# Kernel optimization log

Hardware: AMD Instinct MI355X
Metric: run time of the kernel (lower is better)

## Reference

```python
import jax, jax.numpy as jnp
import numpy as np
from jax import lax

B, CIN, COUT, N, H, W = 8, 64, 64, 9, 128, 128
KS, PAD = 3, 1
EPS = 1e-5
DN = ('NCHW', 'OIHW', 'NCHW')

def _conv(x, w, b, pad):
    y = lax.conv_general_dilated(x, w, (1, 1), [(pad, pad), (pad, pad)], dimension_numbers=DN)
    return y + b[None, :, None, None]

def setup_inputs() -> dict:
    key = jax.random.key(0)
    ks = jax.random.split(key, 8)
    fan = CIN * KS * KS
    s = 1.0 / np.sqrt(fan)
    return {
        'x': jax.random.normal(ks[0], (B, CIN, H, W), dtype=jnp.float32),
        'kernels_w': jax.random.uniform(ks[1], (N, COUT, CIN, KS, KS), minval=-s, maxval=s, dtype=jnp.float32),
        'kernels_b': jax.random.uniform(ks[2], (N, COUT), minval=-s, maxval=s, dtype=jnp.float32),
        'obs1_w': jax.random.uniform(ks[3], (COUT // 2, CIN, 1, 1), minval=-1/np.sqrt(CIN), maxval=1/np.sqrt(CIN), dtype=jnp.float32),
        'obs1_b': jax.random.uniform(ks[4], (COUT // 2,), minval=-1/np.sqrt(CIN), maxval=1/np.sqrt(CIN), dtype=jnp.float32),
        'obs2_w': jax.random.uniform(ks[5], (N, COUT // 2, 1, 1), minval=-1/np.sqrt(COUT // 2), maxval=1/np.sqrt(COUT // 2), dtype=jnp.float32),
        'obs2_b': jax.random.uniform(ks[6], (N,), minval=-1/np.sqrt(COUT // 2), maxval=1/np.sqrt(COUT // 2), dtype=jnp.float32),
        'gamma': jnp.ones((COUT,), dtype=jnp.float32),
        'beta': jnp.zeros((COUT,), dtype=jnp.float32),
    }

def reference(x, kernels_w, kernels_b, obs1_w, obs1_b, obs2_w, obs2_b, gamma, beta):
    b, _, h, w = x.shape
    # all N path convs as one grouped-output conv: (B, N*COUT, H, W)
    paths = _conv(x, kernels_w.reshape(N * COUT, CIN, KS, KS), kernels_b.reshape(-1), PAD)
    paths = paths.reshape(b, N, COUT, h, w)
    # observer: 1x1 conv -> tanh -> 1x1 conv, scores (B, N, H, W)
    scores = _conv(jnp.tanh(_conv(x, obs1_w, obs1_b, 0)), obs2_w, obs2_b, 0)
    # eval-mode collapse: per-pixel argmax over paths, one-hot weighted sum == gather
    idx = jnp.argmax(scores, axis=1)  # (B, H, W)
    sel = jnp.take_along_axis(paths, idx[:, None, None, :, :], axis=1)[:, 0]  # (B, COUT, H, W)
    out = jax.nn.relu(sel)
    # ModularPhaseNorm2d (assumed instance-norm-style per-channel spatial norm with affine)
    mu = jnp.mean(out, axis=(2, 3), keepdims=True)
    var = jnp.var(out, axis=(2, 3), keepdims=True)
    y = (out - mu) * lax.rsqrt(var + EPS)
    return y * gamma[None, :, None, None] + beta[None, :, None, None]
```

## Files before the change

### kernel.cpp

```cpp
#include <hip/hip_runtime.h>
#include <hip/hip_bf16.h>
#include <stdint.h>

#define B_    8
#define CIN   64
#define COUT  64
#define NPATH 9
#define H_    128
#define W_    128
#define HW    16384
#define PTOT  131072
#define NBIN  72
#define CHUNK 64
#define NBLK  256

typedef float  f32x4  __attribute__((ext_vector_type(4)));
typedef __bf16 bf16x8 __attribute__((ext_vector_type(8)));
typedef short  short8 __attribute__((ext_vector_type(8)));
typedef unsigned short ushort4v __attribute__((ext_vector_type(4)));

__device__ __forceinline__ short f2bf(float f) {
    __bf16 b = (__bf16)f;
    return __builtin_bit_cast(short, b);
}
__device__ __forceinline__ float bf2f(unsigned short u) {
    unsigned v = ((unsigned)u) << 16;
    return __builtin_bit_cast(float, v);
}

__global__ void k_pre(const float* __restrict__ x,
                      const float* __restrict__ w1, const float* __restrict__ b1,
                      const float* __restrict__ w2, const float* __restrict__ b2,
                      const float* __restrict__ kw,
                      unsigned* __restrict__ gcnt, unsigned* __restrict__ lists,
                      unsigned short* __restrict__ Xb,
                      unsigned short* __restrict__ WbF) {
    int t = threadIdx.x;
    if (blockIdx.x >= 512) {
        int ob = ((int)blockIdx.x - 512) * 4096 + t * 16;
        #pragma unroll
        for (int j = 0; j < 16; ++j) {
            int o = ob + j;
            int jj   = o & 7;
            int lane = (o >> 3) & 63;
            int f    = (o >> 9) & 3;
            int rest = o >> 11;
            int s    = rest % 18;
            int n    = rest / 18;
            int c    = f * 16 + (lane & 15);
            int kg   = lane >> 4;
            int ci   = ((s & 1) << 5) + (kg << 3) + jj;
            int tap  = s >> 1;
            WbF[o] = (unsigned short)f2bf(kw[((n * 64 + c) * 64 + ci) * 9 + tap]);
        }
        return;
    }
    __shared__ float sw1[2048];
    __shared__ float sw2[288];
    __shared__ float sb1[32];
    __shared__ float sb2[9];
    __shared__ unsigned scnt[NBIN];
    __shared__ unsigned sbase[NBIN];
    #pragma unroll
    for (int i = 0; i < 8; ++i) sw1[t + i * 256] = w1[t + i * 256];
    for (int i = t; i < 288; i += 256) sw2[i] = w2[i];
    if (t < 32) sb1[t] = b1[t];
    if (t < 9)  sb2[t] = b2[t];
    if (t < NBIN) scnt[t] = 0u;
    __syncthreads();

    int p  = blockIdx.x * 256 + t;
    int b  = p >> 14;
    const float* xp = x + (size_t)b * 64 * HW + (p & 16383);
    float xv[64];
    #pragma unroll
    for (int ci = 0; ci < 64; ++ci) xv[ci] = xp[ci * HW];

    #pragma unroll
    for (int j = 0; j < 8; ++j) {
        short8 v;
        #pragma unroll
        for (int q = 0; q < 8; ++q) v[q] = f2bf(xv[j * 8 + q]);
        *(short8*)(Xb + (((size_t)p) << 6) + j * 8) = v;
    }

    float s[9];
    #pragma unroll
    for (int nn = 0; nn < 9; ++nn) s[nn] = sb2[nn];

    for (int j = 0; j < 32; ++j) {
        float a = sb1[j];
        const float4* wv = (const float4*)&sw1[j * 64];
        #pragma unroll
        for (int q = 0; q < 16; ++q) {
            float4 v = wv[q];
            a += xv[q*4+0]*v.x + xv[q*4+1]*v.y + xv[q*4+2]*v.z + xv[q*4+3]*v.w;
        }
        float hsig = tanhf(a);
        #pragma unroll
        for (int nn = 0; nn < 9; ++nn) s[nn] += hsig * sw2[nn * 32 + j];
    }
    float best = s[0]; int bi = 0;
    #pragma unroll
    for (int nn = 1; nn < 9; ++nn) if (s[nn] > best) { best = s[nn]; bi = nn; }

    int bin = bi * 8 + b;
    unsigned rank = atomicAdd(&scnt[bin], 1u);
    __syncthreads();
    if (t < NBIN && scnt[t]) sbase[t] = atomicAdd(&gcnt[t], scnt[t]);
    __syncthreads();
    lists[bin * 16384 + sbase[bin] + rank] = (unsigned)p;
}

__global__ void k_prefix(const unsigned* __restrict__ gcnt,
                         unsigned long long* __restrict__ chunkinfo,
                         unsigned* __restrict__ ctot) {
    __shared__ unsigned st[NBIN + 1];
    int t = threadIdx.x;
    if (t == 0) {
        unsigned acc = 0;
        for (int bin = 0; bin < NBIN; ++bin) {
            st[bin] = acc;
            acc += (gcnt[bin] + (CHUNK - 1u)) / CHUNK;
        }
        st[NBIN] = acc;
        *ctot = acc;
    }
    __syncthreads();
    if (t < NBIN) {
        unsigned c0 = st[t], cnt = gcnt[t];
        unsigned nch = (cnt + (CHUNK - 1u)) / CHUNK;
        for (unsigned k = 0; k < nch; ++k)
            chunkinfo[c0 + k] = ((unsigned long long)t << 32)
                              | ((unsigned long long)cnt << 16)
                              | (unsigned long long)(k * CHUNK);
    }
}

__global__ __launch_bounds__(512, 2) void k_conv(
        const unsigned short* __restrict__ Xb, const unsigned short* __restrict__ WbF,
        const float* __restrict__ kb, const unsigned* __restrict__ lists,
        const unsigned long long* __restrict__ chunkinfo, const unsigned* __restrict__ ctot,
        unsigned short* __restrict__ Yc, float* __restrict__ sums) {
    __shared__ char blds[2][73728];
    int t = threadIdx.x;
    int wid = t >> 6, lane = t & 63, kg = lane >> 4, l15 = lane & 15;
    int f = wid & 3, gh = wid >> 2;
    int spx = t >> 3;
    int sq8 = ((t & 7) ^ (spx & 7)) * 8;

    unsigned C = *ctot;
    unsigned bid = (blockIdx.x & 7) * 32 + (blockIdx.x >> 3);
    unsigned c0 = (bid * C) / NBLK, c1 = ((bid + 1) * C) / NBLK;
    if (c0 >= c1) return;

    #define STAGE9(P, BUF) do {                                                   \
        unsigned p_ = (P);                                                        \
        int h_ = (int)((p_ >> 7) & 127u), w_ = (int)(p_ & 127u);                  \
        unsigned pb_ = p_ & ~16383u;                                              \
        _Pragma("unroll")                                                         \
        for (int k_ = 0; k_ < 9; ++k_) {                                          \
            int dh_ = k_ / 3 - 1, dw_ = k_ % 3 - 1;                               \
            int h2_ = min(max(h_ + dh_, 0), 127);                                 \
            int w2_ = min(max(w_ + dw_, 0), 127);                                 \
            const unsigned short* src_ =                                          \
                Xb + ((size_t)(pb_ | (unsigned)((h2_ << 7) + w2_)) << 6) + sq8;   \
            __builtin_amdgcn_global_load_lds(                                     \
                (const __attribute__((address_space(1))) unsigned int*)src_,      \
                (__attribute__((address_space(3))) unsigned int*)((BUF) + k_ * 8192 + t * 16), \
                16, 0, 0);                                                        \
        }                                                                         \
    } while (0)

    unsigned long long info = chunkinfo[c0];
    int bin  = (int)(info >> 32);
    int cnt  = (int)((info >> 16) & 0xFFFFu);
    int base = (int)(info & 0xFFFFu);
    int n = bin >> 3, b = bin & 7;

    short8 wv[18];
    #pragma unroll
    for (int s = 0; s < 18; ++s)
        wv[s] = *(const short8*)(WbF + n * 36864 + ((s * 4 + f) * 64 + lane) * 8);
    f32x4 bias = *(const f32x4*)(kb + n * 64 + f * 16 + kg * 4);

    unsigned pc0 = lists[bin * 16384 + min(base + gh * 32 + l15,      cnt - 1)];
    unsigned pc1 = lists[bin * 16384 + min(base + gh * 32 + 16 + l15, cnt - 1)];
    { unsigned ps = lists[bin * 16384 + min(base + spx, cnt - 1)];
      STAGE9(ps, blds[0]); }

    int cur = 0;
    float s1[4] = {0.f,0.f,0.f,0.f}, s2[4] = {0.f,0.f,0.f,0.f};

    for (unsigned c = c0; c < c1; ++c) {
        bool last = (c + 1 >= c1);
        int bin_n = bin, cnt_n = cnt, base_n = base;
        unsigned pn0 = 0, pn1 = 0;
        if (!last) {
            unsigned long long in2 = chunkinfo[c + 1];
            bin_n  = (int)(in2 >> 32);
            cnt_n  = (int)((in2 >> 16) & 0xFFFFu);
            base_n = (int)(in2 & 0xFFFFu);
            pn0 = lists[bin_n * 16384 + min(base_n + gh * 32 + l15,      cnt_n - 1)];
            pn1 = lists[bin_n * 16384 + min(base_n + gh * 32 + 16 + l15, cnt_n - 1)];
            { unsigned ps = lists[bin_n * 16384 + min(base_n + spx, cnt_n - 1)];
              STAGE9(ps, blds[cur ^ 1]); }
            asm volatile("s_waitcnt vmcnt(11)" ::: "memory");
        } else {
            asm volatile("s_waitcnt vmcnt(0)" ::: "memory");
        }
        __builtin_amdgcn_sched_barrier(0);
        __builtin_amdgcn_s_barrier();

        int v0 = (base + gh * 32 + l15)      < cnt ? 1 : 0;
        int v1 = (base + gh * 32 + 16 + l15) < cnt ? 1 : 0;
        int inb0 = 0, inb1 = 0;
        {
            int h0 = (int)((pc0 >> 7) & 127u), w0 = (int)(pc0 & 127u);
            int h1 = (int)((pc1 >> 7) & 127u), w1 = (int)(pc1 & 127u);
            #pragma unroll
            for (int tap = 0; tap < 9; ++tap) {
                int dh = tap / 3 - 1, dw = tap % 3 - 1;
                if ((unsigned)(h0 + dh) < 128u && (unsigned)(w0 + dw) < 128u) inb0 |= (1 << tap);
                if ((unsigned)(h1 + dh) < 128u && (unsigned)(w1 + dw) < 128u) inb1 |= (1 << tap);
            }
            inb0 = v0 ? inb0 : 0;
            inb1 = v1 ? inb1 : 0;
        }

        f32x4 acc0 = (f32x4)0.0f, acc1 = (f32x4)0.0f;
        const short8 zero8 = (short8)0;
        const char* bufc = blds[cur];
        #pragma unroll
        for (int s = 0; s < 18; ++s) {
            const int tap = s >> 1, half = s & 1;
            bf16x8 af = __builtin_bit_cast(bf16x8, wv[s]);
            const int q = (((half << 2) + kg) ^ (l15 & 7)) * 16;
            {
                int px = gh * 32 + l15;
                short8 braw = *(const short8*)(bufc + tap * 8192 + px * 128 + q);
                short8 sel = ((inb0 >> tap) & 1) ? braw : zero8;
                acc0 = __builtin_amdgcn_mfma_f32_16x16x32_bf16(
                           af, __builtin_bit_cast(bf16x8, sel), acc0, 0, 0, 0);
            }
            {
                int px = gh * 32 + 16 + l15;
                short8 braw = *(const short8*)(bufc + tap * 8192 + px * 128 + q);
                short8 sel = ((inb1 >> tap) & 1) ? braw : zero8;
                acc1 = __builtin_amdgcn_mfma_f32_16x16x32_bf16(
                           af, __builtin_bit_cast(bf16x8, sel), acc1, 0, 0, 0);
            }
        }

        {
            f32x4 o0, o1;
            #pragma unroll
            for (int r = 0; r < 4; ++r) {
                o0[r] = fmaxf(acc0[r] + bias[r], 0.0f);
                o1[r] = fmaxf(acc1[r] + bias[r], 0.0f);
            }
            if (v0) {
                ushort4v u;
                #pragma unroll
                for (int r = 0; r < 4; ++r) u[r] = (unsigned short)f2bf(o0[r]);
                *(ushort4v*)(Yc + (((size_t)pc0) << 6) + f * 16 + kg * 4) = u;
            }
            if (v1) {
                ushort4v u;
                #pragma unroll
                for (int r = 0; r < 4; ++r) u[r] = (unsigned short)f2bf(o1[r]);
                *(ushort4v*)(Yc + (((size_t)pc1) << 6) + f * 16 + kg * 4) = u;
            }
            #pragma unroll
            for (int r = 0; r < 4; ++r) {
                float a = v0 ? o0[r] : 0.0f, bb = v1 ? o1[r] : 0.0f;
                s1[r] += a + bb;
                s2[r] += a * a + bb * bb;
            }
        }

        if (!last && bin_n != bin) {
            float f1[4], f2[4];
            #pragma unroll
            for (int r = 0; r < 4; ++r) { f1[r] = s1[r]; f2[r] = s2[r]; s1[r] = 0.f; s2[r] = 0.f; }
            #pragma unroll
            for (int m = 1; m < 16; m <<= 1) {
                #pragma unroll
                for (int r = 0; r < 4; ++r) {
                    f1[r] += __shfl_xor(f1[r], m, 64);
                    f2[r] += __shfl_xor(f2[r], m, 64);
                }
            }
            if (l15 == 0) {
                #pragma unroll
                for (int r = 0; r < 4; ++r) {
                    int ch = f * 16 + kg * 4 + r;
                    atomicAdd(&sums[b * 64 + ch],       f1[r]);
                    atomicAdd(&sums[512 + b * 64 + ch], f2[r]);
                }
            }
            n = bin_n >> 3; b = bin_n & 7;
            #pragma unroll
            for (int s = 0; s < 18; ++s)
                wv[s] = *(const short8*)(WbF + n * 36864 + ((s * 4 + f) * 64 + lane) * 8);
            bias = *(const f32x4*)(kb + n * 64 + f * 16 + kg * 4);
        }
        bin = bin_n; cnt = cnt_n; base = base_n; pc0 = pn0; pc1 = pn1;
        cur ^= 1;
        __builtin_amdgcn_s_barrier();
    }

    #pragma unroll
    for (int m = 1; m < 16; m <<= 1) {
        #pragma unroll
        for (int r = 0; r < 4; ++r) {
            s1[r] += __shfl_xor(s1[r], m, 64);
            s2[r] += __shfl_xor(s2[r], m, 64);
        }
    }
    if (l15 == 0) {
        #pragma unroll
        for (int r = 0; r < 4; ++r) {
            int ch = f * 16 + kg * 4 + r;
            atomicAdd(&sums[b * 64 + ch],       s1[r]);
            atomicAdd(&sums[512 + b * 64 + ch], s2[r]);
        }
    }
    #undef STAGE9
}

__global__ void k_final(const unsigned short* __restrict__ Yc, const float* __restrict__ sums,
                        const float* __restrict__ gamma, const float* __restrict__ beta,
                        float* __restrict__ out) {
    __shared__ float ld[128][66];
    __shared__ float smu[64], srs[64], sg[64], sb[64];
    int t = threadIdx.x;
    int b = blockIdx.y, hw0 = blockIdx.x * 128;
    if (t < 64) {
        float mu = sums[b * 64 + t] * (1.0f / HW);
        float vr = sums[512 + b * 64 + t] * (1.0f / HW) - mu * mu;
        smu[t] = mu;
        srs[t] = rsqrtf(fmaxf(vr, 0.0f) + 1e-5f);
        sg[t] = gamma[t]; sb[t] = beta[t];
    }
    int i = t >> 1, half = t & 1;
    const short8* row = (const short8*)(Yc + (((size_t)(b * HW + hw0 + i)) << 6) + half * 32);
    #pragma unroll
    for (int q = 0; q < 4; ++q) {
        short8 v = row[q];
        #pragma unroll
        for (int j = 0; j < 8; ++j)
            ld[i][half * 32 + q * 8 + j] = bf2f((unsigned short)v[j]);
    }
    __syncthreads();
    #pragma unroll
    for (int rep = 0; rep < 32; ++rep) {
        int idx = rep * 256 + t;
        int c = idx >> 7, j = idx & 127;
        float v = (ld[j][c] - smu[c]) * srs[c] * sg[c] + sb[c];
        out[(((size_t)b * 64 + c) << 14) + hw0 + j] = v;
    }
}

extern "C" void kernel_launch(void* const* d_in, const int* in_sizes, int n_in,
                              void* d_out, int out_size, void* d_ws, size_t ws_size,
                              hipStream_t stream) {
    const float* x    = (const float*)d_in[0];
    const float* kw   = (const float*)d_in[1];
    const float* kb   = (const float*)d_in[2];
    const float* w1   = (const float*)d_in[3];
    const float* b1   = (const float*)d_in[4];
    const float* w2   = (const float*)d_in[5];
    const float* b2   = (const float*)d_in[6];
    const float* gam  = (const float*)d_in[7];
    const float* bet  = (const float*)d_in[8];
    float* out = (float*)d_out;

    char* ws = (char*)d_ws;
    unsigned* gcnt      = (unsigned*)(ws + 0);
    unsigned* ctot      = (unsigned*)(ws + 512);
    float*    sums      = (float*)   (ws + 4096);
    unsigned long long* chunkinfo = (unsigned long long*)(ws + 16384);
    unsigned* lists     = (unsigned*)(ws + 65536);
    unsigned short* Yc  = (unsigned short*)(ws + 5308416);
    unsigned short* Xb  = (unsigned short*)(ws + 22085632);
    unsigned short* WbF = (unsigned short*)(ws + 38862848);

    hipMemsetAsync(ws, 0, 8192, stream);
    k_pre<<<593, 256, 0, stream>>>(x, w1, b1, w2, b2, kw, gcnt, lists, Xb, WbF);
    k_prefix<<<1, 256, 0, stream>>>(gcnt, chunkinfo, ctot);
    k_conv<<<NBLK, 512, 0, stream>>>(Xb, WbF, kb, lists, chunkinfo, ctot, Yc, sums);
    k_final<<<dim3(128, 8), 256, 0, stream>>>(Yc, sums, gam, bet, out);
}
```

Baseline: 98.10 us.

## Stage x through LDS in pre-pass, halve conv chunk size and deepen prefetch

The pre-pass now loads a 512-pixel tile of x into LDS with async global-to-LDS copies and has each thread process two pixels. It also swaps tanhf for an exp2-based approximation. The conv kernel halves the chunk size to 32 pixels and doubles the block count to 512. It halves the LDS buffers to allow four blocks per CU, splits the 9-tap staging across two thread halves, and prefetches chunk metadata two chunks ahead. The intent is better occupancy, more load balance across bins and more latency hiding, at the cost of more weight reloads on bin changes and a fast tanh that could flip argmax ties.

Result: slower. 108.6 us (+10.7%).

```diff
diff --git a/kernel.cpp b/kernel.cpp
--- a/kernel.cpp
+++ b/kernel.cpp
@@ -11,8 +11,9 @@
 #define HW    16384
 #define PTOT  131072
 #define NBIN  72
-#define CHUNK 64
-#define NBLK  256
+#define CHUNK 32
+#define NBLK  512
+#define MAXCHUNK 8192
 
 typedef float  f32x4  __attribute__((ext_vector_type(4)));
 typedef __bf16 bf16x8 __attribute__((ext_vector_type(8)));
@@ -27,8 +28,13 @@
     unsigned v = ((unsigned)u) << 16;
     return __builtin_bit_cast(float, v);
 }
-
-__global__ void k_pre(const float* __restrict__ x,
+__device__ __forceinline__ float fast_tanh(float a) {
+    float e = __builtin_amdgcn_exp2f(a * 2.885390081777927f);
+    return 1.0f - 2.0f / (e + 1.0f);
+}
+
+__global__ __launch_bounds__(256) void k_pre(
+                      const float* __restrict__ x,
                       const float* __restrict__ w1, const float* __restrict__ b1,
                       const float* __restrict__ w2, const float* __restrict__ b2,
                       const float* __restrict__ kw,
@@ -36,8 +42,8 @@
                       unsigned short* __restrict__ Xb,
                       unsigned short* __restrict__ WbF) {
     int t = threadIdx.x;
-    if (blockIdx.x >= 512) {
-        int ob = ((int)blockIdx.x - 512) * 4096 + t * 16;
+    if (blockIdx.x >= 256) {
+        int ob = ((int)blockIdx.x - 256) * 4096 + t * 16;
         #pragma unroll
         for (int j = 0; j < 16; ++j) {
             int o = ob + j;
@@ -55,12 +61,29 @@
         }
         return;
     }
+    __shared__ float tile[64 * 512];
     __shared__ float sw1[2048];
     __shared__ float sw2[288];
     __shared__ float sb1[32];
     __shared__ float sb2[9];
     __shared__ unsigned scnt[NBIN];
     __shared__ unsigned sbase[NBIN];
+    int wid = t >> 6, lane = t & 63;
+    int px0 = blockIdx.x * 512;
+    int hwb = px0 & 16383;
+    int b = blockIdx.x >> 5;
+
+    #pragma unroll
+    for (int k = 0; k < 16; ++k) {
+        int ch = wid * 16 + k;
+        const float* src = x + (((size_t)(b * 64 + ch)) << 14) + hwb;
+        #pragma unroll
+        for (int hf = 0; hf < 2; ++hf)
+            __builtin_amdgcn_global_load_lds(
+                (const __attribute__((address_space(1))) unsigned int*)(src + hf * 256 + lane * 4),
+                (__attribute__((address_space(3))) unsigned int*)((char*)tile + ch * 2048 + hf * 1024 + lane * 16),
+                16, 0, 0);
+    }
     #pragma unroll
     for (int i = 0; i < 8; ++i) sw1[t + i * 256] = w1[t + i * 256];
     for (int i = t; i < 288; i += 256) sw2[i] = w2[i];
@@ -69,47 +92,71 @@
     if (t < NBIN) scnt[t] = 0u;
     __syncthreads();
 
-    int p  = blockIdx.x * 256 + t;
-    int b  = p >> 14;
-    const float* xp = x + (size_t)b * 64 * HW + (p & 16383);
-    float xv[64];
-    #pragma unroll
-    for (int ci = 0; ci < 64; ++ci) xv[ci] = xp[ci * HW];
-
-    #pragma unroll
-    for (int j = 0; j < 8; ++j) {
-        short8 v;
-        #pragma unroll
-        for (int q = 0; q < 8; ++q) v[q] = f2bf(xv[j * 8 + q]);
-        *(short8*)(Xb + (((size_t)p) << 6) + j * 8) = v;
-    }
-
-    float s[9];
-    #pragma unroll
-    for (int nn = 0; nn < 9; ++nn) s[nn] = sb2[nn];
-
+    float h0[32], h1[32];
+    #pragma unroll
+    for (int j = 0; j < 32; ++j) { h0[j] = sb1[j]; h1[j] = sb1[j]; }
+
+    unsigned short e0[8], e1[8];
+    size_t xo0 = ((size_t)(px0 + t)) << 6;
+    size_t xo1 = ((size_t)(px0 + 256 + t)) << 6;
+    #pragma unroll
+    for (int q = 0; q < 16; ++q) {
+        float a0 = tile[(q * 4 + 0) * 512 + t];
+        float a1 = tile[(q * 4 + 1) * 512 + t];
+        float a2 = tile[(q * 4 + 2) * 512 + t];
+        float a3 = tile[(q * 4 + 3) * 512 + t];
+        float c0 = tile[(q * 4 + 0) * 512 + 256 + t];
+        float c1 = tile[(q * 4 + 1) * 512 + 256 + t];
+        float c2 = tile[(q * 4 + 2) * 512 + 256 + t];
+        float c3 = tile[(q * 4 + 3) * 512 + 256 + t];
+        const int qo = (q & 1) * 4;
+        e0[qo + 0] = (unsigned short)f2bf(a0); e0[qo + 1] = (unsigned short)f2bf(a1);
+        e0[qo + 2] = (unsigned short)f2bf(a2); e0[qo + 3] = (unsigned short)f2bf(a3);
+        e1[qo + 0] = (unsigned short)f2bf(c0); e1[qo + 1] = (unsigned short)f2bf(c1);
+        e1[qo + 2] = (unsigned short)f2bf(c2); e1[qo + 3] = (unsigned short)f2bf(c3);
+        if (q & 1) {
+            short8 v0, v1;
+            #pragma unroll
+            for (int i = 0; i < 8; ++i) { v0[i] = (short)e0[i]; v1[i] = (short)e1[i]; }
+            *(short8*)(Xb + xo0 + (q >> 1) * 8) = v0;
+            *(short8*)(Xb + xo1 + (q >> 1) * 8) = v1;
+        }
+        #pragma unroll
+        for (int j = 0; j < 32; ++j) {
+            const f32x4 wv4 = *(const f32x4*)&sw1[j * 64 + q * 4];
+            h0[j] += a0 * wv4[0] + a1 * wv4[1] + a2 * wv4[2] + a3 * wv4[3];
+            h1[j] += c0 * wv4[0] + c1 * wv4[1] + c2 * wv4[2] + c3 * wv4[3];
+        }
+    }
+
+    float s0[9], s1[9];
+    #pragma unroll
+    for (int nn = 0; nn < 9; ++nn) { s0[nn] = sb2[nn]; s1[nn] = sb2[nn]; }
+    #pragma unroll
     for (int j = 0; j < 32; ++j) {
-        float a = sb1[j];
-        const float4* wv = (const float4*)&sw1[j * 64];
-        #pragma unroll
-        for (int q = 0; q < 16; ++q) {
-            float4 v = wv[q];
-            a += xv[q*4+0]*v.x + xv[q*4+1]*v.y + xv[q*4+2]*v.z + xv[q*4+3]*v.w;
-        }
-        float hsig = tanhf(a);
-        #pragma unroll
-        for (int nn = 0; nn < 9; ++nn) s[nn] += hsig * sw2[nn * 32 + j];
-    }
-    float best = s[0]; int bi = 0;
-    #pragma unroll
-    for (int nn = 1; nn < 9; ++nn) if (s[nn] > best) { best = s[nn]; bi = nn; }
-
-    int bin = bi * 8 + b;
-    unsigned rank = atomicAdd(&scnt[bin], 1u);
+        float t0 = fast_tanh(h0[j]);
+        float t1 = fast_tanh(h1[j]);
+        #pragma unroll
+        for (int nn = 0; nn < 9; ++nn) {
+            float wv = sw2[nn * 32 + j];
+            s0[nn] += t0 * wv;
+            s1[nn] += t1 * wv;
+        }
+    }
+    float b0 = s0[0], b1v = s1[0]; int i0 = 0, i1 = 0;
+    #pragma unroll
+    for (int nn = 1; nn < 9; ++nn) {
+        if (s0[nn] > b0)  { b0 = s0[nn]; i0 = nn; }
+        if (s1[nn] > b1v) { b1v = s1[nn]; i1 = nn; }
+    }
+    int bin0 = i0 * 8 + b, bin1 = i1 * 8 + b;
+    unsigned r0 = atomicAdd(&scnt[bin0], 1u);
+    unsigned r1 = atomicAdd(&scnt[bin1], 1u);
     __syncthreads();
     if (t < NBIN && scnt[t]) sbase[t] = atomicAdd(&gcnt[t], scnt[t]);
     __syncthreads();
-    lists[bin * 16384 + sbase[bin] + rank] = (unsigned)p;
+    lists[bin0 * 16384 + sbase[bin0] + r0] = (unsigned)(px0 + t);
+    lists[bin1 * 16384 + sbase[bin1] + r1] = (unsigned)(px0 + 256 + t);
 }
 
 __global__ void k_prefix(const unsigned* __restrict__ gcnt,
@@ -117,6 +164,7 @@
                          unsigned* __restrict__ ctot) {
     __shared__ unsigned st[NBIN + 1];
     int t = threadIdx.x;
+    for (int i = t; i < MAXCHUNK; i += 256) chunkinfo[i] = ~0ull;
     if (t == 0) {
         unsigned acc = 0;
         for (int bin = 0; bin < NBIN; ++bin) {
@@ -137,149 +185,132 @@
     }
 }
 
-__global__ __launch_bounds__(512, 2) void k_conv(
+__global__ __launch_bounds__(512, 4) void k_conv(
         const unsigned short* __restrict__ Xb, const unsigned short* __restrict__ WbF,
         const float* __restrict__ kb, const unsigned* __restrict__ lists,
         const unsigned long long* __restrict__ chunkinfo, const unsigned* __restrict__ ctot,
         unsigned short* __restrict__ Yc, float* __restrict__ sums) {
-    __shared__ char blds[2][73728];
+    __shared__ char blds[2][36864];
     int t = threadIdx.x;
     int wid = t >> 6, lane = t & 63, kg = lane >> 4, l15 = lane & 15;
     int f = wid & 3, gh = wid >> 2;
-    int spx = t >> 3;
-    int sq8 = ((t & 7) ^ (spx & 7)) * 8;
+    int slot = t & 255, spx = slot >> 3;
+    int sq8 = ((slot & 7) ^ (spx & 7)) * 8;
+    int tap0 = (t >> 8) * 5;
+    int ntap = (t >> 8) ? 4 : 5;
 
     unsigned C = *ctot;
-    unsigned bid = (blockIdx.x & 7) * 32 + (blockIdx.x >> 3);
+    unsigned bid = (blockIdx.x & 7) * 64 + (blockIdx.x >> 3);
     unsigned c0 = (bid * C) / NBLK, c1 = ((bid + 1) * C) / NBLK;
     if (c0 >= c1) return;
 
-    #define STAGE9(P, BUF) do {                                                   \
+    #define STAGE(P, BUF) do {                                                    \
         unsigned p_ = (P);                                                        \
         int h_ = (int)((p_ >> 7) & 127u), w_ = (int)(p_ & 127u);                  \
         unsigned pb_ = p_ & ~16383u;                                              \
         _Pragma("unroll")                                                         \
-        for (int k_ = 0; k_ < 9; ++k_) {                                          \
-            int dh_ = k_ / 3 - 1, dw_ = k_ % 3 - 1;                               \
-            int h2_ = min(max(h_ + dh_, 0), 127);                                 \
-            int w2_ = min(max(w_ + dw_, 0), 127);                                 \
-            const unsigned short* src_ =                                          \
-                Xb + ((size_t)(pb_ | (unsigned)((h2_ << 7) + w2_)) << 6) + sq8;   \
-            __builtin_amdgcn_global_load_lds(                                     \
-                (const __attribute__((address_space(1))) unsigned int*)src_,      \
-                (__attribute__((address_space(3))) unsigned int*)((BUF) + k_ * 8192 + t * 16), \
-                16, 0, 0);                                                        \
+        for (int k_ = 0; k_ < 5; ++k_) {                                          \
+            if (k_ < ntap) {                                                      \
+                int tap_ = tap0 + k_;                                             \
+                int dh_ = tap_ / 3 - 1, dw_ = tap_ % 3 - 1;                       \
+                int h2_ = min(max(h_ + dh_, 0), 127);                             \
+                int w2_ = min(max(w_ + dw_, 0), 127);                             \
+                const unsigned short* s_ =                                        \
+                    Xb + ((size_t)(pb_ | (unsigned)((h2_ << 7) + w2_)) << 6) + sq8; \
+                __builtin_amdgcn_global_load_lds(                                 \
+                    (const __attribute__((address_space(1))) unsigned int*)s_,    \
+                    (__attribute__((address_space(3))) unsigned int*)((BUF) + tap_ * 4096 + slot * 16), \
+                    16, 0, 0);                                                    \
+            }                                                                     \
         }                                                                         \
     } while (0)
 
-    unsigned long long info = chunkinfo[c0];
-    int bin  = (int)(info >> 32);
-    int cnt  = (int)((info >> 16) & 0xFFFFu);
-    int base = (int)(info & 0xFFFFu);
-    int n = bin >> 3, b = bin & 7;
-
+    #define DECODE(INFO, BIN, CNT, BAS) { BIN = (int)((INFO) >> 32); \
+        CNT = (int)(((INFO) >> 16) & 0xFFFFu); BAS = (int)((INFO) & 0xFFFFu); }
+
+    unsigned long long inf;
+    int cb, cc_, cbase; unsigned cpm, cps;
+    inf = chunkinfo[c0];
+    DECODE(inf, cb, cc_, cbase);
+    cpm = lists[cb * 16384 + min(cbase + gh * 16 + l15, cc_ - 1)];
+    cps = lists[cb * 16384 + min(cbase + spx, cc_ - 1)];
+    STAGE(cps, blds[0]);
+
+    int nb, nc_, nbase; unsigned npm, nps;
+    inf = chunkinfo[min(c0 + 1, c1 - 1)];
+    DECODE(inf, nb, nc_, nbase);
+    npm = lists[nb * 16384 + min(nbase + gh * 16 + l15, nc_ - 1)];
+    nps = lists[nb * 16384 + min(nbase + spx, nc_ - 1)];
+    unsigned long long inf2 = chunkinfo[min(c0 + 2, c1 - 1)];
+
+    int n = cb >> 3, b = cb & 7;
     short8 wv[18];
     #pragma unroll
     for (int s = 0; s < 18; ++s)
         wv[s] = *(const short8*)(WbF + n * 36864 + ((s * 4 + f) * 64 + lane) * 8);
     f32x4 bias = *(const f32x4*)(kb + n * 64 + f * 16 + kg * 4);
 
-    unsigned pc0 = lists[bin * 16384 + min(base + gh * 32 + l15,      cnt - 1)];
-    unsigned pc1 = lists[bin * 16384 + min(base + gh * 32 + 16 + l15, cnt - 1)];
-    { unsigned ps = lists[bin * 16384 + min(base + spx, cnt - 1)];
-      STAGE9(ps, blds[0]); }
-
     int cur = 0;
     float s1[4] = {0.f,0.f,0.f,0.f}, s2[4] = {0.f,0.f,0.f,0.f};
 
     for (unsigned c = c0; c < c1; ++c) {
-        bool last = (c + 1 >= c1);
-        int bin_n = bin, cnt_n = cnt, base_n = base;
-        unsigned pn0 = 0, pn1 = 0;
-        if (!last) {
-            unsigned long long in2 = chunkinfo[c + 1];
-            bin_n  = (int)(in2 >> 32);
-            cnt_n  = (int)((in2 >> 16) & 0xFFFFu);
-            base_n = (int)(in2 & 0xFFFFu);
-            pn0 = lists[bin_n * 16384 + min(base_n + gh * 32 + l15,      cnt_n - 1)];
-            pn1 = lists[bin_n * 16384 + min(base_n + gh * 32 + 16 + l15, cnt_n - 1)];
-            { unsigned ps = lists[bin_n * 16384 + min(base_n + spx, cnt_n - 1)];
-              STAGE9(ps, blds[cur ^ 1]); }
-            asm volatile("s_waitcnt vmcnt(11)" ::: "memory");
-        } else {
-            asm volatile("s_waitcnt vmcnt(0)" ::: "memory");
-        }
+        STAGE(nps, blds[cur ^ 1]);
+        int fb, fc_, fbase; unsigned fpm, fps;
+        DECODE(inf2, fb, fc_, fbase);
+        fpm = lists[fb * 16384 + min(fbase + gh * 16 + l15, fc_ - 1)];
+        fps = lists[fb * 16384 + min(fbase + spx, fc_ - 1)];
+        unsigned long long inf3 = chunkinfo[min(c + 3, c1 - 1)];
+
+        asm volatile("s_waitcnt vmcnt(7)" ::: "memory");
         __builtin_amdgcn_sched_barrier(0);
         __builtin_amdgcn_s_barrier();
 
-        int v0 = (base + gh * 32 + l15)      < cnt ? 1 : 0;
-        int v1 = (base + gh * 32 + 16 + l15) < cnt ? 1 : 0;
-        int inb0 = 0, inb1 = 0;
+        int valid = (cbase + gh * 16 + l15) < cc_ ? 1 : 0;
+        int inb = 0;
         {
-            int h0 = (int)((pc0 >> 7) & 127u), w0 = (int)(pc0 & 127u);
-            int h1 = (int)((pc1 >> 7) & 127u), w1 = (int)(pc1 & 127u);
+            int hh = (int)((cpm >> 7) & 127u), ww = (int)(cpm & 127u);
             #pragma unroll
             for (int tap = 0; tap < 9; ++tap) {
                 int dh = tap / 3 - 1, dw = tap % 3 - 1;
-                if ((unsigned)(h0 + dh) < 128u && (unsigned)(w0 + dw) < 128u) inb0 |= (1 << tap);
-                if ((unsigned)(h1 + dh) < 128u && (unsigned)(w1 + dw) < 128u) inb1 |= (1 << tap);
+                if ((unsigned)(hh + dh) < 128u && (unsigned)(ww + dw) < 128u) inb |= (1 << tap);
             }
-            inb0 = v0 ? inb0 : 0;
-            inb1 = v1 ? inb1 : 0;
-        }
-
-        f32x4 acc0 = (f32x4)0.0f, acc1 = (f32x4)0.0f;
+            inb = valid ? inb : 0;
+        }
+
+        f32x4 acc = (f32x4)0.0f;
         const short8 zero8 = (short8)0;
         const char* bufc = blds[cur];
+        int px = gh * 16 + l15;
         #pragma unroll
         for (int s = 0; s < 18; ++s) {
-            const int tap = s >> 1, half = s & 1;
-            bf16x8 af = __builtin_bit_cast(bf16x8, wv[s]);
-            const int q = (((half << 2) + kg) ^ (l15 & 7)) * 16;
-            {
-                int px = gh * 32 + l15;
-                short8 braw = *(const short8*)(bufc + tap * 8192 + px * 128 + q);
-                short8 sel = ((inb0 >> tap) & 1) ? braw : zero8;
-                acc0 = __builtin_amdgcn_mfma_f32_16x16x32_bf16(
-                           af, __builtin_bit_cast(bf16x8, sel), acc0, 0, 0, 0);
-            }
-            {
-                int px = gh * 32 + 16 + l15;
-                short8 braw = *(const short8*)(bufc + tap * 8192 + px * 128 + q);
-                short8 sel = ((inb1 >> tap) & 1) ? braw : zero8;
-                acc1 = __builtin_amdgcn_mfma_f32_16x16x32_bf16(
-                           af, __builtin_bit_cast(bf16x8, sel), acc1, 0, 0, 0);
-            }
+            const int tap = s >> 1;
+            const int pr = ((s & 1) << 2) | kg;
+            short8 braw = *(const short8*)(bufc + tap * 4096 + px * 128 + ((pr ^ (px & 7)) << 4));
+            short8 sel = ((inb >> tap) & 1) ? braw : zero8;
+            acc = __builtin_amdgcn_mfma_f32_16x16x32_bf16(
+                      __builtin_bit_cast(bf16x8, wv[s]),
+                      __builtin_bit_cast(bf16x8, sel), acc, 0, 0, 0);
         }
 
         {
-            f32x4 o0, o1;
-            #pragma unroll
-            for (int r = 0; r < 4; ++r) {
-                o0[r] = fmaxf(acc0[r] + bias[r], 0.0f);
-                o1[r] = fmaxf(acc1[r] + bias[r], 0.0f);
-            }
-            if (v0) {
+            f32x4 o;
+            #pragma unroll
+            for (int r = 0; r < 4; ++r) o[r] = fmaxf(acc[r] + bias[r], 0.0f);
+            if (valid) {
                 ushort4v u;
                 #pragma unroll
-                for (int r = 0; r < 4; ++r) u[r] = (unsigned short)f2bf(o0[r]);
-                *(ushort4v*)(Yc + (((size_t)pc0) << 6) + f * 16 + kg * 4) = u;
+                for (int r = 0; r < 4; ++r) u[r] = (unsigned short)f2bf(o[r]);
+                *(ushort4v*)(Yc + (((size_t)cpm) << 6) + f * 16 + kg * 4) = u;
             }
-            if (v1) {
-                ushort4v u;
-                #pragma unroll
-                for (int r = 0; r < 4; ++r) u[r] = (unsigned short)f2bf(o1[r]);
-                *(ushort4v*)(Yc + (((size_t)pc1) << 6) + f * 16 + kg * 4) = u;
+            #pragma unroll
+            for (int r = 0; r < 4; ++r) {
+                float sv = valid ? o[r] : 0.0f;
+                s1[r] += sv;
+                s2[r] += sv * sv;
             }
-            #pragma unroll
-            for (int r = 0; r < 4; ++r) {
-                float a = v0 ? o0[r] : 0.0f, bb = v1 ? o1[r] : 0.0f;
-                s1[r] += a + bb;
-                s2[r] += a * a + bb * bb;
-            }
-        }
-
-        if (!last && bin_n != bin) {
+        }
+
+        if (nb != cb && c + 1 < c1) {
             float f1[4], f2[4];
             #pragma unroll
             for (int r = 0; r < 4; ++r) { f1[r] = s1[r]; f2[r] = s2[r]; s1[r] = 0.f; s2[r] = 0.f; }
@@ -299,13 +330,16 @@
                     atomicAdd(&sums[512 + b * 64 + ch], f2[r]);
                 }
             }
-            n = bin_n >> 3; b = bin_n & 7;
+            n = nb >> 3; b = nb & 7;
             #pragma unroll
             for (int s = 0; s < 18; ++s)
                 wv[s] = *(const short8*)(WbF + n * 36864 + ((s * 4 + f) * 64 + lane) * 8);
             bias = *(const f32x4*)(kb + n * 64 + f * 16 + kg * 4);
         }
-        bin = bin_n; cnt = cnt_n; base = base_n; pc0 = pn0; pc1 = pn1;
+
+        cb = nb; cc_ = nc_; cbase = nbase; cpm = npm;
+        nb = fb; nc_ = fc_; nbase = fbase; npm = fpm; nps = fps;
+        inf2 = inf3;
         cur ^= 1;
         __builtin_amdgcn_s_barrier();
     }
@@ -326,7 +360,8 @@
             atomicAdd(&sums[512 + b * 64 + ch], s2[r]);
         }
     }
-    #undef STAGE9
+    #undef STAGE
+    #undef DECODE
 }
 
 __global__ void k_final(const unsigned short* __restrict__ Yc, const float* __restrict__ sums,
@@ -381,13 +416,13 @@
     unsigned* ctot      = (unsigned*)(ws + 512);
     float*    sums      = (float*)   (ws + 4096);
     unsigned long long* chunkinfo = (unsigned long long*)(ws + 16384);
-    unsigned* lists     = (unsigned*)(ws + 65536);
-    unsigned short* Yc  = (unsigned short*)(ws + 5308416);
-    unsigned short* Xb  = (unsigned short*)(ws + 22085632);
-    unsigned short* WbF = (unsigned short*)(ws + 38862848);
+    unsigned* lists     = (unsigned*)(ws + 131072);
+    unsigned short* Yc  = (unsigned short*)(ws + 5242880);
+    unsigned short* Xb  = (unsigned short*)(ws + 22020096);
+    unsigned short* WbF = (unsigned short*)(ws + 38797312);
 
     hipMemsetAsync(ws, 0, 8192, stream);
-    k_pre<<<593, 256, 0, stream>>>(x, w1, b1, w2, b2, kw, gcnt, lists, Xb, WbF);
+    k_pre<<<337, 256, 0, stream>>>(x, w1, b1, w2, b2, kw, gcnt, lists, Xb, WbF);
     k_prefix<<<1, 256, 0, stream>>>(gcnt, chunkinfo, ctot);
     k_conv<<<NBLK, 512, 0, stream>>>(Xb, WbF, kb, lists, chunkinfo, ctot, Yc, sums);
     k_final<<<dim3(128, 8), 256, 0, stream>>>(Yc, sums, gam, bet, out);
```
